# Performance work log

Hardware: AMD Instinct MI355X
Metric: run time of the kernel (lower is better)

The kernel has to match this reference:

```python
import jax, jax.numpy as jnp
import numpy as np


def setup_inputs() -> dict:
    key = jax.random.key(0)
    k1, k2, k3, k4 = jax.random.split(key, 4)
    b, h, t, dim, topk = 16, 8, 196, 512, 49
    x = jax.random.normal(k1, (b, t, dim), dtype=jnp.float32)
    adj = jax.random.normal(k2, (b, h, t, t), dtype=jnp.float32)  # per-head routing logits
    Wqkv = jax.random.normal(k3, (dim, 3 * dim), dtype=jnp.float32) * 0.02
    Wv = jax.random.normal(k4, (dim, dim), dtype=jnp.float32) * 0.02
    return {"x": x, "adj": adj, "Wqkv": Wqkv, "Wv": Wv, "topk": topk}


def reference(x, adj, Wqkv, Wv, topk):
    b, t, dim = x.shape
    h = adj.shape[1]
    d = dim // h
    scale = dim ** (-0.5)  # note: full dim, matching source (self.scale = dim**-0.5)

    # qkv projection (stand-in for GIN conv_proj_qkv with nhid = 3*dim)
    qkv = (x @ Wqkv).reshape(b, t, h, 3 * d).transpose(0, 2, 1, 3)  # b h t 3d
    q, k, v = jnp.split(qkv, 3, axis=-1)  # each b h t d

    # TopkRouting: indices of top-k routing logits per (b, h, query-token)
    _, r_idx = jax.lax.top_k(adj, topk)  # b h t topk (r_weight unused: mul_weight='none')

    # KGather: irregular gather of concatenated k/v rows per query token
    kv = jnp.concatenate([k, v], axis=-1).reshape(b * h, t, 2 * d)
    idx = r_idx.reshape(b * h, t, topk)
    kv_sel = jax.vmap(lambda m, i: m[i])(kv, idx)          # (bh, t, topk, 2d)
    kv_sel = kv_sel.reshape(b, h, t, topk, 2 * d)
    k_sel, v_sel = jnp.split(kv_sel, 2, axis=-1)            # b h t topk d

    # small-window attention: each query attends to its topk gathered rows (w^2 = 1)
    attn = jax.nn.softmax(jnp.einsum('bhtd,bhtkd->bhtk', q * scale, k_sel), axis=-1)
    o = jnp.einsum('bhtk,bhtkd->bhtd', attn, v_sel)

    o = o.transpose(0, 2, 1, 3).reshape(b, t, dim)
    o = jax.nn.gelu(o, approximate=False)  # torch F.gelu default = exact erf
    return o @ Wv
```

## Files before the change

kernel.cpp:

```cpp
#include <hip/hip_runtime.h>
#include <hip/hip_bf16.h>
#include <cmath>

#define B_   16
#define H_   8
#define T_   196
#define DIM_ 512
#define DHEAD_ 64
#define TOPK_ 49
#define BT_  (B_ * T_)
#define BH_  (B_ * H_)

#define QB_OFF   0u
#define KB_OFF   1605632u
#define VT_OFF   3211264u
#define XB_OFF   5046272u
#define WQKVT_OFF 6651904u
#define WVT_OFF  7438336u
#define MASK_OFF 7700480u

typedef __bf16 bf16x8 __attribute__((ext_vector_type(8)));
typedef float f32x4 __attribute__((ext_vector_type(4)));

__device__ __forceinline__ unsigned short f2bf(float f) {
    union { float f; unsigned int u; } v; v.f = f;
    const unsigned int u = v.u;
    return (unsigned short)((u + 0x7FFFu + ((u >> 16) & 1u)) >> 16);
}

__device__ __forceinline__ unsigned int ordered_u32(float f) {
    int i = __float_as_int(f);
    return (i < 0) ? ~(unsigned int)i : ((unsigned int)i | 0x80000000u);
}

__device__ __forceinline__ void gload16(const void* g, void* l) {
    __builtin_amdgcn_global_load_lds(
        (const __attribute__((address_space(1))) unsigned int*)g,
        (__attribute__((address_space(3))) unsigned int*)l, 16, 0, 0);
}

__device__ __forceinline__ void route_topk_q(const float* __restrict__ adj,
                                             unsigned int* __restrict__ masks,
                                             const int q, const int lane) {
    const float* arow = adj + (size_t)q * T_;
    const bool v3 = (lane < 4);
    unsigned int u[4];
    u[0] = ordered_u32(arow[lane]);
    u[1] = ordered_u32(arow[lane + 64]);
    u[2] = ordered_u32(arow[lane + 128]);
    u[3] = v3 ? ordered_u32(arow[lane + 192]) : 0u;

    unsigned int prefix = 0u, thr = 0u;
    int k = TOPK_, A = T_;
    for (int b = 31; b >= 0; --b) {
        int C1 = 0;
        C1 += __popcll(__ballot(((u[0] ^ prefix) >> b) == 1u));
        C1 += __popcll(__ballot(((u[1] ^ prefix) >> b) == 1u));
        C1 += __popcll(__ballot(((u[2] ^ prefix) >> b) == 1u));
        C1 += __popcll(__ballot(((u[3] ^ prefix) >> b) == 1u));
        if (C1 >= k) { prefix |= (1u << b); A = C1; }
        else { k -= C1; A -= C1; }

        if (k == A || k == 1) {
            const bool mx = (k == 1);
            unsigned int best = mx ? 0u : 0xFFFFFFFFu;
#pragma unroll
            for (int s2 = 0; s2 < 4; ++s2) {
                const bool valid = (s2 < 3) || v3;
                const bool act = valid && (((u[s2] ^ prefix) >> b) == 0u);
                if (act) best = mx ? (u[s2] > best ? u[s2] : best)
                                   : (u[s2] < best ? u[s2] : best);
            }
#pragma unroll
            for (int off = 32; off >= 1; off >>= 1) {
                const unsigned int o = __shfl_xor(best, off);
                best = mx ? (o > best ? o : best) : (o < best ? o : best);
            }
            thr = best;
            break;
        }
        if (b == 0) thr = prefix;
    }

    const unsigned long long lmask = (1ull << lane) - 1ull;
    unsigned long long gm[4];
    int G = 0;
#pragma unroll
    for (int s2 = 0; s2 < 4; ++s2) {
        const bool valid = (s2 < 3) || v3;
        gm[s2] = __ballot(valid && (u[s2] > thr));
        G += __popcll(gm[s2]);
    }
    const int need = TOPK_ - G;
    int cum = 0;
    unsigned long long sb0 = 0, sb1 = 0, sb2 = 0, sb3 = 0;
#pragma unroll
    for (int s2 = 0; s2 < 4; ++s2) {
        const bool valid = (s2 < 3) || v3;
        const bool e = valid && (u[s2] == thr);
        const unsigned long long em = __ballot(e);
        const int rk = cum + __popcll(em & lmask);
        cum += __popcll(em);
        const unsigned long long sel = gm[s2] | __ballot(e && (rk < need));
        if (s2 == 0) sb0 = sel; else if (s2 == 1) sb1 = sel;
        else if (s2 == 2) sb2 = sel; else sb3 = sel;
    }
    if (lane < 8) {
        const unsigned long long mv = (lane < 2) ? sb0 : (lane < 4) ? sb1
                                    : (lane < 6) ? sb2 : sb3;
        const unsigned int wd = (lane & 1) ? (unsigned int)(mv >> 32) : (unsigned int)mv;
        masks[(size_t)q * 8 + lane] = wd;
    }
}

__global__ __launch_bounds__(256) void prep(const float* __restrict__ x,
                                            const float* __restrict__ Wqkv,
                                            unsigned short* __restrict__ xb,
                                            unsigned short* __restrict__ wqkvT) {
    __shared__ unsigned short Tt[64][72];
    const int t = threadIdx.x;
    const int bid = blockIdx.x;

    if (bid < 784) {
        const size_t base = ((size_t)bid * 256 + t) * 8;
        const float4 v0 = *(const float4*)&x[base];
        const float4 v1 = *(const float4*)&x[base + 4];
        uint4 pk;
        pk.x = (unsigned int)f2bf(v0.x) | ((unsigned int)f2bf(v0.y) << 16);
        pk.y = (unsigned int)f2bf(v0.z) | ((unsigned int)f2bf(v0.w) << 16);
        pk.z = (unsigned int)f2bf(v1.x) | ((unsigned int)f2bf(v1.y) << 16);
        pk.w = (unsigned int)f2bf(v1.z) | ((unsigned int)f2bf(v1.w) << 16);
        *(uint4*)&xb[base] = pk;
        return;
    }

    const int b = bid - 784;
    const int tx = b % 24, ty = b / 24;
    const int c0 = tx * 64, r0 = ty * 64;
#pragma unroll
    for (int p = 0; p < 4; ++p) {
        const int r = (t >> 4) + 16 * p;
        const int cl = (t & 15) * 4;
        const float4 v = *(const float4*)&Wqkv[(size_t)(r0 + r) * 1536 + c0 + cl];
        Tt[cl + 0][r] = f2bf(v.x);
        Tt[cl + 1][r] = f2bf(v.y);
        Tt[cl + 2][r] = f2bf(v.z);
        Tt[cl + 3][r] = f2bf(v.w);
    }
    __syncthreads();
#pragma unroll
    for (int p = 0; p < 2; ++p) {
        const int cc = (t >> 3) + 32 * p;
        const int ch = (t & 7) * 8;
        *(uint4*)&wqkvT[(size_t)(c0 + cc) * 512 + r0 + ch] = *(const uint4*)&Tt[cc][ch];
    }
}

template <int BN, int MODE, int FUSE, typename CT>
__global__ __launch_bounds__(256) void gemm_mfma(const unsigned short* __restrict__ A,
                                                 const unsigned short* __restrict__ Bt,
                                                 CT* __restrict__ C,
                                                 const int M, const int N, const int K,
                                                 const float* __restrict__ adj,
                                                 unsigned int* __restrict__ masks,
                                                 unsigned short* __restrict__ vT,
                                                 const float* __restrict__ Wv,
                                                 unsigned short* __restrict__ wvT) {
    constexpr int FN = BN / 32;
    constexpr int CSZ = (MODE == 1) ? 64 * 132 : 1;
    struct ABt { unsigned short A[64][32]; unsigned short B[BN][32]; };
    __shared__ union {
        ABt ab;
        unsigned short Cs[CSZ];
        unsigned short Tt[FUSE ? 64 : 1][72];
    } sm;

    const int tid = threadIdx.x;
    const int lane = tid & 63, wid = tid >> 6;
    const int mt = M >> 6;
    const int nGemm = mt * (N / BN);
    const int bid = blockIdx.x;

    if constexpr (FUSE) {
        if (bid >= nGemm) {
            const int rid = bid - nGemm;
            if (rid < 6272) {
                route_topk_q(adj, masks, rid * 4 + wid, lane);
            } else if (rid < 6300) {
                const int e0 = (rid - 6272) * 8192 + tid;
#pragma unroll
                for (int i = 0; i < 32; ++i) {
                    const int e = e0 + i * 256;
                    const int bh = e / 1792;
                    const int rem = e - bh * 1792;
                    const int d = rem / 28;
                    const int tt = rem - d * 28;
                    vT[(size_t)bh * (64 * 224) + (size_t)d * 224 + 196 + tt] = 0;
                }
            } else {
                const int b = rid - 6300;
                const int tx = b & 7, ty = b >> 3;
                const int c0 = tx * 64, r0 = ty * 64;
#pragma unroll
                for (int p = 0; p < 4; ++p) {
                    const int r = (tid >> 4) + 16 * p;
                    const int cl = (tid & 15) * 4;
                    const float4 v = *(const float4*)&Wv[(size_t)(r0 + r) * 512 + c0 + cl];
                    sm.Tt[cl + 0][r] = f2bf(v.x);
                    sm.Tt[cl + 1][r] = f2bf(v.y);
                    sm.Tt[cl + 2][r] = f2bf(v.z);
                    sm.Tt[cl + 3][r] = f2bf(v.w);
                }
                __syncthreads();
#pragma unroll
                for (int p = 0; p < 2; ++p) {
                    const int cc = (tid >> 3) + 32 * p;
                    const int ch = (tid & 7) * 8;
                    *(uint4*)&wvT[(size_t)(c0 + cc) * 512 + r0 + ch] =
                        *(const uint4*)&sm.Tt[cc][ch];
                }
            }
            return;
        }
    }

    const int bx = bid % mt;
    const int by = bid / mt;
    const int row0 = bx * 64;
    const int col0 = by * BN;
    const int wr = wid >> 1, wc = wid & 1;

    f32x4 acc[2][FN];
#pragma unroll
    for (int m = 0; m < 2; ++m)
#pragma unroll
        for (int n = 0; n < FN; ++n)
            acc[m][n] = (f32x4){0.0f, 0.0f, 0.0f, 0.0f};

    const int srow = lane >> 2;
    const int scol = (lane & 3) * 8;
    const unsigned short* aSrc = A + (size_t)(row0 + wid * 16 + srow) * K + scol;
    const unsigned short* bSrc = Bt + (size_t)(col0 + wid * 16 + srow) * K + scol;
    const unsigned short* bSrc2 = bSrc + (size_t)64 * K;
    unsigned short* ldsA = &sm.ab.A[wid * 16][0];
    unsigned short* ldsB = &sm.ab.B[wid * 16][0];
    unsigned short* ldsB2 = &sm.ab.B[(BN == 128 ? 64 : 0) + wid * 16][0];

    const int fr = lane & 15;
    const int fk8 = (lane >> 4) * 8;

    for (int k0 = 0; k0 < K; k0 += 32) {
        gload16(aSrc, ldsA);
        gload16(bSrc, ldsB);
        if constexpr (BN == 128) gload16(bSrc2, ldsB2);
        aSrc += 32; bSrc += 32; bSrc2 += 32;
        __syncthreads();

        bf16x8 af[2], bfv[FN];
#pragma unroll
        for (int m = 0; m < 2; ++m)
            af[m] = *(const bf16x8*)&sm.ab.A[wr * 32 + m * 16 + fr][fk8];
#pragma unroll
        for (int n = 0; n < FN; ++n)
            bfv[n] = *(const bf16x8*)&sm.ab.B[wc * (BN / 2) + n * 16 + fr][fk8];
#pragma unroll
        for (int m = 0; m < 2; ++m)
#pragma unroll
            for (int n = 0; n < FN; ++n)
                acc[m][n] = __builtin_amdgcn_mfma_f32_16x16x32_bf16(af[m], bfv[n], acc[m][n], 0, 0, 0);
        __syncthreads();
    }

    if constexpr (MODE == 0) {
#pragma unroll
        for (int m = 0; m < 2; ++m)
#pragma unroll
            for (int n = 0; n < FN; ++n)
#pragma unroll
                for (int i = 0; i < 4; ++i) {
                    const int row = row0 + wr * 32 + m * 16 + (lane >> 4) * 4 + i;
                    const int col = col0 + wc * (BN / 2) + n * 16 + (lane & 15);
                    C[(size_t)row * N + col] = (CT)acc[m][n][i];
                }
    } else {
#pragma unroll
        for (int m = 0; m < 2; ++m)
#pragma unroll
            for (int n = 0; n < FN; ++n)
#pragma unroll
                for (int i = 0; i < 4; ++i) {
                    const int rl = wr * 32 + m * 16 + (lane >> 4) * 4 + i;
                    const int cl = wc * (BN / 2) + n * 16 + (lane & 15);
                    sm.Cs[rl * 132 + cl] = f2bf(acc[m][n][i]);
                }
        __syncthreads();

        unsigned short* ubase = (unsigned short*)C;
#pragma unroll
        for (int ch = 0; ch < BN / 64; ++ch) {
            const int abscol = col0 + ch * 64;
            const int which = (abscol >> 6) % 3;
            const int hh = abscol / 192;
            if (which < 2) {
                const int r = tid >> 2;
                const int co = (tid & 3) * 16;
                const int gr = row0 + r;
                const int bb = gr / T_;
                const int tt = gr - bb * T_;
                const uint2 a0 = *(const uint2*)&sm.Cs[r * 132 + ch * 64 + co];
                const uint2 a1 = *(const uint2*)&sm.Cs[r * 132 + ch * 64 + co + 4];
                const uint2 a2 = *(const uint2*)&sm.Cs[r * 132 + ch * 64 + co + 8];
                const uint2 a3 = *(const uint2*)&sm.Cs[r * 132 + ch * 64 + co + 12];
                unsigned short* dst = ubase + (size_t)which * KB_OFF +
                                      ((size_t)(bb * H_ + hh) * T_ + tt) * DHEAD_ + co;
                uint4 w0; w0.x = a0.x; w0.y = a0.y; w0.z = a1.x; w0.w = a1.y;
                uint4 w1; w1.x = a2.x; w1.y = a2.y; w1.z = a3.x; w1.w = a3.y;
                *(uint4*)&dst[0] = w0;
                *(uint4*)&dst[8] = w1;
            } else {
                const int d = tid >> 2;
                const int j0 = (tid & 3) * 16;
                union { unsigned short s[16]; uint2 v2[4]; } tmp;
#pragma unroll
                for (int j = 0; j < 16; ++j)
                    tmp.s[j] = sm.Cs[(j0 + j) * 132 + ch * 64 + d];
                const int gr0 = row0 + j0;
                const int bb0 = gr0 / T_;
                const int bb1 = (gr0 + 15) / T_;
                if (bb0 == bb1) {
                    const int tt = gr0 - bb0 * T_;
                    unsigned short* dst = ubase + VT_OFF +
                                          (size_t)(bb0 * H_ + hh) * (64 * 224) +
                                          (size_t)d * 224 + tt;
                    *(uint2*)&dst[0]  = tmp.v2[0];
                    *(uint2*)&dst[4]  = tmp.v2[1];
                    *(uint2*)&dst[8]  = tmp.v2[2];
                    *(uint2*)&dst[12] = tmp.v2[3];
                } else {
#pragma unroll
                    for (int j = 0; j < 16; ++j) {
                        const int gr = gr0 + j;
                        const int bb = gr / T_;
                        const int tt = gr - bb * T_;
                        ubase[VT_OFF + (size_t)(bb * H_ + hh) * (64 * 224) +
                              (size_t)d * 224 + tt] = tmp.s[j];
                    }
                }
            }
        }
    }
}

__global__ __launch_bounds__(64) void attn_mfma(const unsigned short* __restrict__ qb,
                                                const unsigned short* __restrict__ kb,
                                                const unsigned short* __restrict__ vT,
                                                const unsigned int* __restrict__ masks,
                                                unsigned short* __restrict__ obuf) {
    __shared__ unsigned int mask_lds[16][8];
    __shared__ unsigned short P[16][232];

    const int lane = threadIdx.x;
    const int qt = blockIdx.x;
    const int bh = blockIdx.y;
    const int bb = bh >> 3, hh = bh & 7;
    const int q0 = qt * 16;

#pragma unroll
    for (int s2 = 0; s2 < 2; ++s2) {
        const int e = lane + s2 * 64;
        const int r = e >> 3, wd = e & 7;
        const int t = q0 + r;
        mask_lds[r][wd] = (t < T_) ? masks[((size_t)bh * T_ + t) * 8 + wd] : 0u;
    }
    *(unsigned long long*)&P[lane >> 2][208 + (lane & 3) * 4] = 0ull;
    __syncthreads();

    const int fr = lane & 15;
    const int fk8 = (lane >> 4) * 8;
    const unsigned short* qbh = qb + ((size_t)bh * T_ + q0) * DHEAD_;
    const unsigned short* kbh = kb + (size_t)bh * T_ * DHEAD_;

    const bf16x8 aq0 = *(const bf16x8*)&qbh[fr * 64 + fk8];
    const bf16x8 aq1 = *(const bf16x8*)&qbh[fr * 64 + 32 + fk8];

    f32x4 s[13];
#pragma unroll
    for (int c = 0; c < 13; ++c) s[c] = (f32x4){0.0f, 0.0f, 0.0f, 0.0f};
#pragma unroll
    for (int c = 0; c < 13; ++c) {
        const bf16x8 b0 = *(const bf16x8*)&kbh[(c * 16 + fr) * 64 + fk8];
        const bf16x8 b1 = *(const bf16x8*)&kbh[(c * 16 + fr) * 64 + 32 + fk8];
        s[c] = __builtin_amdgcn_mfma_f32_16x16x32_bf16(aq0, b0, s[c], 0, 0, 0);
        s[c] = __builtin_amdgcn_mfma_f32_16x16x32_bf16(aq1, b1, s[c], 0, 0, 0);
    }

    const float scale = 0.044194173824159216f;
    float l0 = 0, l1 = 0, l2 = 0, l3 = 0;
#pragma unroll
    for (int i = 0; i < 4; ++i) {
        const int rowl = (lane >> 4) * 4 + i;
        float li = 0.0f;
#pragma unroll
        for (int c = 0; c < 13; ++c) {
            const unsigned int mw = mask_lds[rowl][c >> 1];
            const bool sel = (mw >> (((c & 1) << 4) + fr)) & 1u;
            const float pv = sel ? __expf(s[c][i] * scale) : 0.0f;
            P[rowl][c * 16 + fr] = f2bf(pv);
            li += pv;
        }
        if (i == 0) l0 = li; else if (i == 1) l1 = li;
        else if (i == 2) l2 = li; else l3 = li;
    }
#pragma unroll
    for (int off = 8; off >= 1; off >>= 1) {
        l0 += __shfl_xor(l0, off);
        l1 += __shfl_xor(l1, off);
        l2 += __shfl_xor(l2, off);
        l3 += __shfl_xor(l3, off);
    }
    const float rl0 = 1.0f / l0, rl1 = 1.0f / l1, rl2 = 1.0f / l2, rl3 = 1.0f / l3;

    const unsigned short* vbh = vT + (size_t)bh * (64 * 224);
    f32x4 o[4];
#pragma unroll
    for (int n = 0; n < 4; ++n) o[n] = (f32x4){0.0f, 0.0f, 0.0f, 0.0f};
#pragma unroll
    for (int kk = 0; kk < 7; ++kk) {
        const bf16x8 ap = *(const bf16x8*)&P[fr][kk * 32 + fk8];
#pragma unroll
        for (int n = 0; n < 4; ++n) {
            const bf16x8 bv = *(const bf16x8*)&vbh[(n * 16 + fr) * 224 + kk * 32 + fk8];
            o[n] = __builtin_amdgcn_mfma_f32_16x16x32_bf16(ap, bv, o[n], 0, 0, 0);
        }
    }

#pragma unroll
    for (int i = 0; i < 4; ++i) {
        const float rl = (i == 0) ? rl0 : (i == 1) ? rl1 : (i == 2) ? rl2 : rl3;
        const int t = q0 + (lane >> 4) * 4 + i;
        if (t < T_) {
            unsigned short* orow = obuf + ((size_t)(bb * T_ + t)) * DIM_ + hh * DHEAD_;
#pragma unroll
            for (int n = 0; n < 4; ++n) {
                const float ov = o[n][i] * rl;
                const float g = 0.5f * ov * (1.0f + erff(ov * 0.70710678118654752f));
                orow[n * 16 + fr] = f2bf(g);
            }
        }
    }
}

extern "C" void kernel_launch(void* const* d_in, const int* in_sizes, int n_in,
                              void* d_out, int out_size, void* d_ws, size_t ws_size,
                              hipStream_t stream) {
    const float* x    = (const float*)d_in[0];
    const float* adj  = (const float*)d_in[1];
    const float* Wqkv = (const float*)d_in[2];
    const float* Wv   = (const float*)d_in[3];
    float* out = (float*)d_out;
    unsigned short* ub = (unsigned short*)d_ws;

    unsigned short* qb    = ub + QB_OFF;
    unsigned short* kb    = ub + KB_OFF;
    unsigned short* vT    = ub + VT_OFF;
    unsigned short* xb    = ub + XB_OFF;
    unsigned short* wqkvT = ub + WQKVT_OFF;
    unsigned short* wvT   = ub + WVT_OFF;
    unsigned int*   masks = (unsigned int*)(ub + MASK_OFF);

    prep<<<976, 256, 0, stream>>>(x, Wqkv, xb, wqkvT);

    gemm_mfma<128, 1, 1, unsigned short><<<6952, 256, 0, stream>>>(
        xb, wqkvT, ub, BT_, 3 * DIM_, DIM_, adj, masks, vT, Wv, wvT);

    attn_mfma<<<dim3(13, BH_), 64, 0, stream>>>(qb, kb, vT, masks, xb);

    gemm_mfma<64, 0, 0, float><<<392, 256, 0, stream>>>(
        xb, wvT, out, BT_, DIM_, DIM_, nullptr, nullptr, nullptr, nullptr, nullptr);
}
```

Baseline: 67.76 us.

## Double-buffer GEMM LDS tiles, simplify radix-select prefix test, raise MFMA wave priority

The GEMM main loop now keeps two LDS buffers and issues the next K-slice's global-to-LDS loads before computing on the current one, so loads can overlap MFMA work, at the cost of doubling the A/B shared-memory footprint. The top-k radix select keeps pre-XORed copies of the keys, which removes the per-bit XOR with the prefix. The attention kernel raises wave priority around its MFMA loops with s_setprio. These are three unrelated micro-optimisations. The larger LDS union may reduce occupancy.

Measured after the change: 64.20 us. 5.3% less time.

```diff
diff --git a/kernel.cpp b/kernel.cpp
--- a/kernel.cpp
+++ b/kernel.cpp
@@ -50,24 +50,30 @@
     u[2] = ordered_u32(arow[lane + 128]);
     u[3] = v3 ? ordered_u32(arow[lane + 192]) : 0u;
 
+    unsigned int w0 = u[0], w1 = u[1], w2 = u[2], w3 = u[3];
     unsigned int prefix = 0u, thr = 0u;
     int k = TOPK_, A = T_;
     for (int b = 31; b >= 0; --b) {
         int C1 = 0;
-        C1 += __popcll(__ballot(((u[0] ^ prefix) >> b) == 1u));
-        C1 += __popcll(__ballot(((u[1] ^ prefix) >> b) == 1u));
-        C1 += __popcll(__ballot(((u[2] ^ prefix) >> b) == 1u));
-        C1 += __popcll(__ballot(((u[3] ^ prefix) >> b) == 1u));
-        if (C1 >= k) { prefix |= (1u << b); A = C1; }
-        else { k -= C1; A -= C1; }
+        C1 += __popcll(__ballot((w0 >> b) == 1u));
+        C1 += __popcll(__ballot((w1 >> b) == 1u));
+        C1 += __popcll(__ballot((w2 >> b) == 1u));
+        C1 += __popcll(__ballot((w3 >> b) == 1u));
+        if (C1 >= k) {
+            const unsigned int bit = 1u << b;
+            prefix |= bit;
+            w0 ^= bit; w1 ^= bit; w2 ^= bit; w3 ^= bit;
+            A = C1;
+        } else { k -= C1; A -= C1; }
 
         if (k == A || k == 1) {
             const bool mx = (k == 1);
             unsigned int best = mx ? 0u : 0xFFFFFFFFu;
+            const unsigned int ww[4] = {w0, w1, w2, w3};
 #pragma unroll
             for (int s2 = 0; s2 < 4; ++s2) {
                 const bool valid = (s2 < 3) || v3;
-                const bool act = valid && (((u[s2] ^ prefix) >> b) == 0u);
+                const bool act = valid && ((ww[s2] >> b) == 0u);
                 if (act) best = mx ? (u[s2] > best ? u[s2] : best)
                                    : (u[s2] < best ? u[s2] : best);
             }
@@ -170,7 +176,7 @@
     constexpr int CSZ = (MODE == 1) ? 64 * 132 : 1;
     struct ABt { unsigned short A[64][32]; unsigned short B[BN][32]; };
     __shared__ union {
-        ABt ab;
+        ABt ab[2];
         unsigned short Cs[CSZ];
         unsigned short Tt[FUSE ? 64 : 1][72];
     } sm;
@@ -242,34 +248,45 @@
     const unsigned short* aSrc = A + (size_t)(row0 + wid * 16 + srow) * K + scol;
     const unsigned short* bSrc = Bt + (size_t)(col0 + wid * 16 + srow) * K + scol;
     const unsigned short* bSrc2 = bSrc + (size_t)64 * K;
-    unsigned short* ldsA = &sm.ab.A[wid * 16][0];
-    unsigned short* ldsB = &sm.ab.B[wid * 16][0];
-    unsigned short* ldsB2 = &sm.ab.B[(BN == 128 ? 64 : 0) + wid * 16][0];
 
     const int fr = lane & 15;
     const int fk8 = (lane >> 4) * 8;
 
-    for (int k0 = 0; k0 < K; k0 += 32) {
-        gload16(aSrc, ldsA);
-        gload16(bSrc, ldsB);
-        if constexpr (BN == 128) gload16(bSrc2, ldsB2);
-        aSrc += 32; bSrc += 32; bSrc2 += 32;
+#define STAGE(BUF) do {                                                        \
+        gload16(aSrc, &sm.ab[BUF].A[wid * 16][0]);                             \
+        gload16(bSrc, &sm.ab[BUF].B[wid * 16][0]);                             \
+        if constexpr (BN == 128) gload16(bSrc2, &sm.ab[BUF].B[64 + wid * 16][0]); \
+        aSrc += 32; bSrc += 32; bSrc2 += 32;                                   \
+    } while (0)
+
+#define COMPUTE(BUF) do {                                                      \
+        bf16x8 af[2], bfv[FN];                                                 \
+        _Pragma("unroll")                                                      \
+        for (int m = 0; m < 2; ++m)                                            \
+            af[m] = *(const bf16x8*)&sm.ab[BUF].A[wr * 32 + m * 16 + fr][fk8]; \
+        _Pragma("unroll")                                                      \
+        for (int n = 0; n < FN; ++n)                                           \
+            bfv[n] = *(const bf16x8*)&sm.ab[BUF].B[wc * (BN / 2) + n * 16 + fr][fk8]; \
+        _Pragma("unroll")                                                      \
+        for (int m = 0; m < 2; ++m)                                            \
+            _Pragma("unroll")                                                  \
+            for (int n = 0; n < FN; ++n)                                       \
+                acc[m][n] = __builtin_amdgcn_mfma_f32_16x16x32_bf16(af[m], bfv[n], acc[m][n], 0, 0, 0); \
+    } while (0)
+
+    STAGE(0);
+    __syncthreads();
+
+    for (int k0 = 0; k0 < K; k0 += 64) {
+        if (k0 + 32 < K) STAGE(1);
+        COMPUTE(0);
         __syncthreads();
-
-        bf16x8 af[2], bfv[FN];
-#pragma unroll
-        for (int m = 0; m < 2; ++m)
-            af[m] = *(const bf16x8*)&sm.ab.A[wr * 32 + m * 16 + fr][fk8];
-#pragma unroll
-        for (int n = 0; n < FN; ++n)
-            bfv[n] = *(const bf16x8*)&sm.ab.B[wc * (BN / 2) + n * 16 + fr][fk8];
-#pragma unroll
-        for (int m = 0; m < 2; ++m)
-#pragma unroll
-            for (int n = 0; n < FN; ++n)
-                acc[m][n] = __builtin_amdgcn_mfma_f32_16x16x32_bf16(af[m], bfv[n], acc[m][n], 0, 0, 0);
+        if (k0 + 64 < K) STAGE(0);
+        COMPUTE(1);
         __syncthreads();
     }
+#undef STAGE
+#undef COMPUTE
 
     if constexpr (MODE == 0) {
 #pragma unroll
@@ -386,6 +403,7 @@
     f32x4 s[13];
 #pragma unroll
     for (int c = 0; c < 13; ++c) s[c] = (f32x4){0.0f, 0.0f, 0.0f, 0.0f};
+    __builtin_amdgcn_s_setprio(1);
 #pragma unroll
     for (int c = 0; c < 13; ++c) {
         const bf16x8 b0 = *(const bf16x8*)&kbh[(c * 16 + fr) * 64 + fk8];
@@ -393,6 +411,7 @@
         s[c] = __builtin_amdgcn_mfma_f32_16x16x32_bf16(aq0, b0, s[c], 0, 0, 0);
         s[c] = __builtin_amdgcn_mfma_f32_16x16x32_bf16(aq1, b1, s[c], 0, 0, 0);
     }
+    __builtin_amdgcn_s_setprio(0);
 
     const float scale = 0.044194173824159216f;
     float l0 = 0, l1 = 0, l2 = 0, l3 = 0;
@@ -424,6 +443,7 @@
     f32x4 o[4];
 #pragma unroll
     for (int n = 0; n < 4; ++n) o[n] = (f32x4){0.0f, 0.0f, 0.0f, 0.0f};
+    __builtin_amdgcn_s_setprio(1);
 #pragma unroll
     for (int kk = 0; kk < 7; ++kk) {
         const bf16x8 ap = *(const bf16x8*)&P[fr][kk * 32 + fk8];
@@ -433,6 +453,7 @@
             o[n] = __builtin_amdgcn_mfma_f32_16x16x32_bf16(ap, bv, o[n], 0, 0, 0);
         }
     }
+    __builtin_amdgcn_s_setprio(0);
 
 #pragma unroll
     for (int i = 0; i < 4; ++i) {
```
